# Optimization experiments

Hardware: AMD Instinct MI355X
Metric: run time of the kernel (lower is better)

The kernel has to match this reference:

```python
import jax, jax.numpy as jnp
import numpy as np

D = 128   # input_dim / num vars
LEAKY_SLOPE = 0.01  # torch F.leaky_relu default


def setup_inputs() -> dict:
    key = jax.random.key(0)
    ks = jax.random.split(key, 7)
    h, o, b = 64, 2, 8192
    scale = 0.05  # keep activations in a sane range
    return {
        "x": jax.random.normal(ks[0], (b, D), jnp.float32),
        "w0": jax.random.normal(ks[1], (D, h, D), jnp.float32) * scale,
        "w1": jax.random.normal(ks[2], (D, h, h), jnp.float32) * scale,
        "w2": jax.random.normal(ks[3], (D, o, h), jnp.float32) * scale,
        "b0": jax.random.normal(ks[4], (D, h), jnp.float32) * scale,
        "b1": jax.random.normal(ks[5], (D, h), jnp.float32) * scale,
        "b2": jax.random.normal(ks[6], (D, o), jnp.float32) * scale,
    }


def reference(x, w0, w1, w2, b0, b1, b2):
    # adjacency: all-ones minus identity (variable t cannot see itself)
    adj = jnp.ones((D, D), x.dtype) - jnp.eye(D, dtype=x.dtype)  # [j? no: (i,j)] symmetric
    # layer 0: out[b,t,i] = sum_j w0[t,i,j] * adj[j,t] * x[b,j]
    # mask the per-variable weights once, then a single contraction (no (t,i,j,b) intermediate)
    w0m = w0 * adj.T[:, None, :]            # (t,i,j); adj symmetric so adj[j,t]==adj[t,j]
    h = jnp.einsum('tij,bj->bti', w0m, x) + b0
    h = jax.nn.leaky_relu(h, LEAKY_SLOPE)
    # layer 1: per-variable dense
    h = jnp.einsum('tij,btj->bti', w1, h) + b1
    h = jax.nn.leaky_relu(h, LEAKY_SLOPE)
    # layer 2 (output, no nonlinearity)
    out = jnp.einsum('tij,btj->bti', w2, h) + b2  # (b, D, output_dim)
    # torch version returns torch.unbind(out, 1); stacked array carries same values
    return out
```

## Files before the change

### kernel.cpp

```cpp
#include <hip/hip_runtime.h>


typedef __bf16 bf16_t;
typedef __bf16 bf16x8 __attribute__((ext_vector_type(8)));
typedef float  f32x4  __attribute__((ext_vector_type(4)));

#define LEAKY 0.01f

#define XB_OFF   0u
#define W0B_OFF  (2048u*1024u)
#define W1B_OFF  (4096u*1024u)
#define W2B_OFF  (5120u*1024u)

#define W0L   0
#define W1L   16384
#define W2L   24576
#define HL    26624
#define H2L   43008
#define SMEMB 59392

__device__ __forceinline__ void async_copy16(void* lds, const void* g) {
    __builtin_amdgcn_global_load_lds(
        (const __attribute__((address_space(1))) unsigned int*)g,
        (__attribute__((address_space(3))) unsigned int*)lds, 16, 0, 0);
}

__global__ __launch_bounds__(256)
void brickify(const float* __restrict__ x,  const float* __restrict__ w0,
              const float* __restrict__ w1, const float* __restrict__ w2,
              unsigned char* __restrict__ ws)
{
    const int wid  = blockIdx.x * 4 + (threadIdx.x >> 6);
    const int lane = threadIdx.x & 63;
    const int lr = lane & 15, lq = lane >> 4;

    float v[8];
    if (wid < 2048) {
        int bt = wid >> 5, rem = wid & 31, nt = rem >> 2, ks = rem & 3;
        const float* s = x + (size_t)(bt*128 + nt*16 + lr) * 128 + ks*32 + lq*8;
        const float4 a = *(const float4*)s, b = *(const float4*)(s + 4);
        v[0]=a.x; v[1]=a.y; v[2]=a.z; v[3]=a.w;
        v[4]=b.x; v[5]=b.y; v[6]=b.z; v[7]=b.w;
    } else if (wid < 4096) {
        int u = wid - 2048, t = u >> 4, rem = u & 15, it = rem >> 2, ks = rem & 3;
        int k0 = ks*32 + lq*8;
        const float* s = w0 + (size_t)(t*64 + it*16 + lr) * 128 + k0;
        const float4 a = *(const float4*)s, b = *(const float4*)(s + 4);
        v[0]=a.x; v[1]=a.y; v[2]=a.z; v[3]=a.w;
        v[4]=b.x; v[5]=b.y; v[6]=b.z; v[7]=b.w;
        #pragma unroll
        for (int j = 0; j < 8; ++j) if (k0 + j == t) v[j] = 0.f;
    } else if (wid < 5120) {
        int u = wid - 4096, t = u >> 3, rem = u & 7, it = rem >> 1, ks = rem & 1;
        const float* s = w1 + (size_t)(t*64 + it*16 + lr) * 64 + ks*32 + lq*8;
        const float4 a = *(const float4*)s, b = *(const float4*)(s + 4);
        v[0]=a.x; v[1]=a.y; v[2]=a.z; v[3]=a.w;
        v[4]=b.x; v[5]=b.y; v[6]=b.z; v[7]=b.w;
    } else {
        int u = wid - 5120, t = u >> 1, ks = u & 1;
        #pragma unroll
        for (int j = 0; j < 8; ++j) v[j] = 0.f;
        if (lr < 2) {
            const float* s = w2 + (size_t)(t*2 + lr) * 64 + ks*32 + lq*8;
            const float4 a = *(const float4*)s, b = *(const float4*)(s + 4);
            v[0]=a.x; v[1]=a.y; v[2]=a.z; v[3]=a.w;
            v[4]=b.x; v[5]=b.y; v[6]=b.z; v[7]=b.w;
        }
    }
    union { bf16_t h[8]; uint4 q; } pk;
    #pragma unroll
    for (int j = 0; j < 8; ++j) pk.h[j] = (bf16_t)v[j];
    ((uint4*)ws)[(size_t)wid * 64 + lane] = pk.q;
}

__global__ __launch_bounds__(256, 2)
void fused_mlp(const unsigned char* __restrict__ ws,
               const float* __restrict__ b0, const float* __restrict__ b1,
               const float* __restrict__ b2, float* __restrict__ out)
{
    __shared__ __align__(1024) unsigned char smem[SMEMB];
    const int tid  = threadIdx.x;
    const int w    = tid >> 6;
    const int lane = tid & 63;
    const int lr = lane & 15, lq = lane >> 4;
    const int bt = blockIdx.x;
    const int t  = blockIdx.y;

    bf16x8 xf[2][4];
    #pragma unroll
    for (int ntl = 0; ntl < 2; ++ntl) {
        int ntg = w * 2 + ntl;
        #pragma unroll
        for (int ks = 0; ks < 4; ++ks)
            xf[ntl][ks] = *(const bf16x8*)(ws + XB_OFF
                            + (size_t)(((bt*8 + ntg)*4 + ks) * 1024) + lane*16);
    }
    f32x4 b0q[4], b1q[4];
    #pragma unroll
    for (int it = 0; it < 4; ++it) {
        b0q[it] = *(const f32x4*)(b0 + t*64 + it*16 + lq*4);
        b1q[it] = *(const f32x4*)(b1 + t*64 + it*16 + lq*4);
    }
    const float2 b2v = *(const float2*)(b2 + t*2);

    for (int c = w; c < 26; c += 4) {
        const unsigned char* g;
        if (c < 16)      g = ws + W0B_OFF + (size_t)t*16384 + c*1024;
        else if (c < 24) g = ws + W1B_OFF + (size_t)t*8192  + (c-16)*1024;
        else             g = ws + W2B_OFF + (size_t)t*2048  + (c-24)*1024;
        async_copy16(smem + c*1024 + lane*16, g + lane*16);
    }
    __syncthreads();

    bf16x8 w0f[4][4];
    #pragma unroll
    for (int it = 0; it < 4; ++it)
        #pragma unroll
        for (int ks = 0; ks < 4; ++ks)
            w0f[it][ks] = *(const bf16x8*)(smem + W0L + (it*4+ks)*1024 + lane*16);

    f32x4 acc0[2][4];
    #pragma unroll
    for (int a = 0; a < 2; ++a)
        #pragma unroll
        for (int b = 0; b < 4; ++b) acc0[a][b] = (f32x4){0.f,0.f,0.f,0.f};

    #pragma unroll
    for (int ks = 0; ks < 4; ++ks)
        #pragma unroll
        for (int it = 0; it < 4; ++it)
            #pragma unroll
            for (int ntl = 0; ntl < 2; ++ntl)
                acc0[ntl][it] = __builtin_amdgcn_mfma_f32_16x16x32_bf16(
                                    w0f[it][ks], xf[ntl][ks], acc0[ntl][it], 0, 0, 0);

    #pragma unroll
    for (int ntl = 0; ntl < 2; ++ntl)
        #pragma unroll
        for (int it = 0; it < 4; ++it) {
            union { bf16_t h[4]; unsigned long long u; } pk;
            #pragma unroll
            for (int r = 0; r < 4; ++r) {
                float u = acc0[ntl][it][r] + b0q[it][r];
                pk.h[r] = (bf16_t)(u > 0.f ? u : LEAKY * u);
            }
            int off = ((w*2+ntl)*2 + (it>>1)) * 1024
                    + (((it&1)*2 + (lq>>1))*16 + lr) * 16 + (lq&1)*8;
            *(unsigned long long*)(smem + HL + off) = pk.u;
        }

    bf16x8 w1f[4][2], hf[2][2];
    #pragma unroll
    for (int it = 0; it < 4; ++it)
        #pragma unroll
        for (int ks = 0; ks < 2; ++ks)
            w1f[it][ks] = *(const bf16x8*)(smem + W1L + (it*2+ks)*1024 + lane*16);
    #pragma unroll
    for (int ntl = 0; ntl < 2; ++ntl)
        #pragma unroll
        for (int ks = 0; ks < 2; ++ks)
            hf[ntl][ks] = *(const bf16x8*)(smem + HL + ((w*2+ntl)*2 + ks)*1024 + lane*16);

    f32x4 acc1[2][4];
    #pragma unroll
    for (int a = 0; a < 2; ++a)
        #pragma unroll
        for (int b = 0; b < 4; ++b) acc1[a][b] = (f32x4){0.f,0.f,0.f,0.f};

    #pragma unroll
    for (int ks = 0; ks < 2; ++ks)
        #pragma unroll
        for (int it = 0; it < 4; ++it)
            #pragma unroll
            for (int ntl = 0; ntl < 2; ++ntl)
                acc1[ntl][it] = __builtin_amdgcn_mfma_f32_16x16x32_bf16(
                                    w1f[it][ks], hf[ntl][ks], acc1[ntl][it], 0, 0, 0);

    #pragma unroll
    for (int ntl = 0; ntl < 2; ++ntl)
        #pragma unroll
        for (int it = 0; it < 4; ++it) {
            union { bf16_t h[4]; unsigned long long u; } pk;
            #pragma unroll
            for (int r = 0; r < 4; ++r) {
                float u = acc1[ntl][it][r] + b1q[it][r];
                pk.h[r] = (bf16_t)(u > 0.f ? u : LEAKY * u);
            }
            int off = ((w*2+ntl)*2 + (it>>1)) * 1024
                    + (((it&1)*2 + (lq>>1))*16 + lr) * 16 + (lq&1)*8;
            *(unsigned long long*)(smem + H2L + off) = pk.u;
        }

    bf16x8 w2f[2], h2f[2][2];
    #pragma unroll
    for (int ks = 0; ks < 2; ++ks)
        w2f[ks] = *(const bf16x8*)(smem + W2L + ks*1024 + lane*16);
    #pragma unroll
    for (int ntl = 0; ntl < 2; ++ntl)
        #pragma unroll
        for (int ks = 0; ks < 2; ++ks)
            h2f[ntl][ks] = *(const bf16x8*)(smem + H2L + ((w*2+ntl)*2 + ks)*1024 + lane*16);

    f32x4 acc2[2];
    acc2[0] = (f32x4){0.f,0.f,0.f,0.f};
    acc2[1] = (f32x4){0.f,0.f,0.f,0.f};
    #pragma unroll
    for (int ks = 0; ks < 2; ++ks)
        #pragma unroll
        for (int ntl = 0; ntl < 2; ++ntl)
            acc2[ntl] = __builtin_amdgcn_mfma_f32_16x16x32_bf16(
                            w2f[ks], h2f[ntl][ks], acc2[ntl], 0, 0, 0);

    if (lq == 0) {
        #pragma unroll
        for (int ntl = 0; ntl < 2; ++ntl) {
            int row = bt*128 + (w*2+ntl)*16 + lr;
            float2 o2 = { acc2[ntl][0] + b2v.x, acc2[ntl][1] + b2v.y };
            *(float2*)(out + (size_t)row*256 + t*2) = o2;
        }
    }
}

extern "C" void kernel_launch(void* const* d_in, const int* in_sizes, int n_in,
                              void* d_out, int out_size, void* d_ws, size_t ws_size,
                              hipStream_t stream) {
    const float* x  = (const float*)d_in[0];
    const float* w0 = (const float*)d_in[1];
    const float* w1 = (const float*)d_in[2];
    const float* w2 = (const float*)d_in[3];
    const float* b0 = (const float*)d_in[4];
    const float* b1 = (const float*)d_in[5];
    const float* b2 = (const float*)d_in[6];
    unsigned char* ws = (unsigned char*)d_ws;
    float* out = (float*)d_out;

    brickify<<<dim3(1344), dim3(256), 0, stream>>>(x, w0, w1, w2, ws);
    fused_mlp<<<dim3(64, 128), dim3(256), 0, stream>>>(ws, b0, b1, b2, out);
}
```

Baseline: 123.6 us.

## Keep per-variable weights in registers and loop blocks over eight batch tiles

The fused MLP kernel now loads each variable's weight fragments straight from global memory into registers once and reuses them across eight batch tiles per block. Previously every block staged the weights through LDS for a single tile. The grid shrinks from 64x128 to 8x128 blocks, and the next tile's x fragments are prefetched while the current tile computes. Biases are folded into the accumulator initialisation and leaky ReLU uses fmaxf. LDS drops to one 16 KB activation buffer, but fewer blocks means less parallelism. The higher register pressure could also cut occupancy, and reusing one LDS buffer for h and h2 without barriers relies on each wave touching only its own region.

```diff
diff --git a/kernel.cpp b/kernel.cpp
--- a/kernel.cpp
+++ b/kernel.cpp
@@ -11,19 +11,6 @@
 #define W0B_OFF  (2048u*1024u)
 #define W1B_OFF  (4096u*1024u)
 #define W2B_OFF  (5120u*1024u)
-
-#define W0L   0
-#define W1L   16384
-#define W2L   24576
-#define HL    26624
-#define H2L   43008
-#define SMEMB 59392
-
-__device__ __forceinline__ void async_copy16(void* lds, const void* g) {
-    __builtin_amdgcn_global_load_lds(
-        (const __attribute__((address_space(1))) unsigned int*)g,
-        (__attribute__((address_space(3))) unsigned int*)lds, 16, 0, 0);
-}
 
 __global__ __launch_bounds__(256)
 void brickify(const float* __restrict__ x,  const float* __restrict__ w0,
@@ -78,23 +65,33 @@
                const float* __restrict__ b0, const float* __restrict__ b1,
                const float* __restrict__ b2, float* __restrict__ out)
 {
-    __shared__ __align__(1024) unsigned char smem[SMEMB];
+    __shared__ __align__(16) unsigned char hsm[16384];
+
     const int tid  = threadIdx.x;
     const int w    = tid >> 6;
     const int lane = tid & 63;
     const int lr = lane & 15, lq = lane >> 4;
-    const int bt = blockIdx.x;
+    const int g  = blockIdx.x;
     const int t  = blockIdx.y;
 
-    bf16x8 xf[2][4];
-    #pragma unroll
-    for (int ntl = 0; ntl < 2; ++ntl) {
-        int ntg = w * 2 + ntl;
+    const unsigned char* w0p = ws + W0B_OFF + (size_t)t*16384 + lane*16;
+    const unsigned char* w1p = ws + W1B_OFF + (size_t)t*8192  + lane*16;
+    const unsigned char* w2p = ws + W2B_OFF + (size_t)t*2048  + lane*16;
+    bf16x8 w0f[4][4], w1f[4][2], w2f[2];
+    #pragma unroll
+    for (int it = 0; it < 4; ++it)
         #pragma unroll
         for (int ks = 0; ks < 4; ++ks)
-            xf[ntl][ks] = *(const bf16x8*)(ws + XB_OFF
-                            + (size_t)(((bt*8 + ntg)*4 + ks) * 1024) + lane*16);
-    }
+            w0f[it][ks] = *(const bf16x8*)(w0p + (it*4+ks)*1024);
+    #pragma unroll
+    for (int it = 0; it < 4; ++it)
+        #pragma unroll
+        for (int ks = 0; ks < 2; ++ks)
+            w1f[it][ks] = *(const bf16x8*)(w1p + (it*2+ks)*1024);
+    #pragma unroll
+    for (int ks = 0; ks < 2; ++ks)
+        w2f[ks] = *(const bf16x8*)(w2p + ks*1024);
+
     f32x4 b0q[4], b1q[4];
     #pragma unroll
     for (int it = 0; it < 4; ++it) {
@@ -103,120 +100,120 @@
     }
     const float2 b2v = *(const float2*)(b2 + t*2);
 
-    for (int c = w; c < 26; c += 4) {
-        const unsigned char* g;
-        if (c < 16)      g = ws + W0B_OFF + (size_t)t*16384 + c*1024;
-        else if (c < 24) g = ws + W1B_OFF + (size_t)t*8192  + (c-16)*1024;
-        else             g = ws + W2B_OFF + (size_t)t*2048  + (c-24)*1024;
-        async_copy16(smem + c*1024 + lane*16, g + lane*16);
-    }
-    __syncthreads();
-
-    bf16x8 w0f[4][4];
-    #pragma unroll
-    for (int it = 0; it < 4; ++it)
+    const unsigned char* xp = ws + XB_OFF + lane*16;
+    bf16x8 xf[2][4];
+    {
+        const int bt0 = g*8;
+        #pragma unroll
+        for (int ntl = 0; ntl < 2; ++ntl)
+            #pragma unroll
+            for (int ks = 0; ks < 4; ++ks)
+                xf[ntl][ks] = *(const bf16x8*)(xp + (size_t)(((bt0*8 + w*2+ntl)*4 + ks))*1024);
+    }
+
+    for (int s = 0; s < 8; ++s) {
+        const int bt = g*8 + s;
+
+        f32x4 acc0[2][4];
+        #pragma unroll
+        for (int ntl = 0; ntl < 2; ++ntl)
+            #pragma unroll
+            for (int it = 0; it < 4; ++it) acc0[ntl][it] = b0q[it];
+
         #pragma unroll
         for (int ks = 0; ks < 4; ++ks)
-            w0f[it][ks] = *(const bf16x8*)(smem + W0L + (it*4+ks)*1024 + lane*16);
-
-    f32x4 acc0[2][4];
-    #pragma unroll
-    for (int a = 0; a < 2; ++a)
-        #pragma unroll
-        for (int b = 0; b < 4; ++b) acc0[a][b] = (f32x4){0.f,0.f,0.f,0.f};
-
-    #pragma unroll
-    for (int ks = 0; ks < 4; ++ks)
-        #pragma unroll
-        for (int it = 0; it < 4; ++it)
+            #pragma unroll
+            for (int it = 0; it < 4; ++it)
+                #pragma unroll
+                for (int ntl = 0; ntl < 2; ++ntl)
+                    acc0[ntl][it] = __builtin_amdgcn_mfma_f32_16x16x32_bf16(
+                                        w0f[it][ks], xf[ntl][ks], acc0[ntl][it], 0, 0, 0);
+
+        {
+            const int btn = (s < 7) ? bt + 1 : bt;
             #pragma unroll
             for (int ntl = 0; ntl < 2; ++ntl)
-                acc0[ntl][it] = __builtin_amdgcn_mfma_f32_16x16x32_bf16(
-                                    w0f[it][ks], xf[ntl][ks], acc0[ntl][it], 0, 0, 0);
-
-    #pragma unroll
-    for (int ntl = 0; ntl < 2; ++ntl)
-        #pragma unroll
-        for (int it = 0; it < 4; ++it) {
-            union { bf16_t h[4]; unsigned long long u; } pk;
-            #pragma unroll
-            for (int r = 0; r < 4; ++r) {
-                float u = acc0[ntl][it][r] + b0q[it][r];
-                pk.h[r] = (bf16_t)(u > 0.f ? u : LEAKY * u);
+                #pragma unroll
+                for (int ks = 0; ks < 4; ++ks)
+                    xf[ntl][ks] = *(const bf16x8*)(xp + (size_t)(((btn*8 + w*2+ntl)*4 + ks))*1024);
+        }
+
+        #pragma unroll
+        for (int ntl = 0; ntl < 2; ++ntl)
+            #pragma unroll
+            for (int it = 0; it < 4; ++it) {
+                union { bf16_t h[4]; unsigned long long u; } pk;
+                #pragma unroll
+                for (int r = 0; r < 4; ++r) {
+                    float u = acc0[ntl][it][r];
+                    pk.h[r] = (bf16_t)fmaxf(u, LEAKY * u);
+                }
+                int off = ((w*2+ntl)*2 + (it>>1)) * 1024
+                        + (((it&1)*2 + (lq>>1))*16 + lr) * 16 + (lq&1)*8;
+                *(unsigned long long*)(hsm + off) = pk.u;
             }
-            int off = ((w*2+ntl)*2 + (it>>1)) * 1024
-                    + (((it&1)*2 + (lq>>1))*16 + lr) * 16 + (lq&1)*8;
-            *(unsigned long long*)(smem + HL + off) = pk.u;
-        }
-
-    bf16x8 w1f[4][2], hf[2][2];
-    #pragma unroll
-    for (int it = 0; it < 4; ++it)
+
+        bf16x8 hf[2][2];
+        #pragma unroll
+        for (int ntl = 0; ntl < 2; ++ntl)
+            #pragma unroll
+            for (int ks = 0; ks < 2; ++ks)
+                hf[ntl][ks] = *(const bf16x8*)(hsm + ((w*2+ntl)*2 + ks)*1024 + lane*16);
+
+        f32x4 acc1[2][4];
+        #pragma unroll
+        for (int ntl = 0; ntl < 2; ++ntl)
+            #pragma unroll
+            for (int it = 0; it < 4; ++it) acc1[ntl][it] = b1q[it];
+
         #pragma unroll
         for (int ks = 0; ks < 2; ++ks)
-            w1f[it][ks] = *(const bf16x8*)(smem + W1L + (it*2+ks)*1024 + lane*16);
-    #pragma unroll
-    for (int ntl = 0; ntl < 2; ++ntl)
+            #pragma unroll
+            for (int it = 0; it < 4; ++it)
+                #pragma unroll
+                for (int ntl = 0; ntl < 2; ++ntl)
+                    acc1[ntl][it] = __builtin_amdgcn_mfma_f32_16x16x32_bf16(
+                                        w1f[it][ks], hf[ntl][ks], acc1[ntl][it], 0, 0, 0);
+
+        #pragma unroll
+        for (int ntl = 0; ntl < 2; ++ntl)
+            #pragma unroll
+            for (int it = 0; it < 4; ++it) {
+                union { bf16_t h[4]; unsigned long long u; } pk;
+                #pragma unroll
+                for (int r = 0; r < 4; ++r) {
+                    float u = acc1[ntl][it][r];
+                    pk.h[r] = (bf16_t)fmaxf(u, LEAKY * u);
+                }
+                int off = ((w*2+ntl)*2 + (it>>1)) * 1024
+                        + (((it&1)*2 + (lq>>1))*16 + lr) * 16 + (lq&1)*8;
+                *(unsigned long long*)(hsm + off) = pk.u;
+            }
+
+        bf16x8 h2f[2][2];
+        #pragma unroll
+        for (int ntl = 0; ntl < 2; ++ntl)
+            #pragma unroll
+            for (int ks = 0; ks < 2; ++ks)
+                h2f[ntl][ks] = *(const bf16x8*)(hsm + ((w*2+ntl)*2 + ks)*1024 + lane*16);
+
+        f32x4 acc2[2];
+        acc2[0] = (f32x4){0.f,0.f,0.f,0.f};
+        acc2[1] = (f32x4){0.f,0.f,0.f,0.f};
         #pragma unroll
         for (int ks = 0; ks < 2; ++ks)
-            hf[ntl][ks] = *(const bf16x8*)(smem + HL + ((w*2+ntl)*2 + ks)*1024 + lane*16);
-
-    f32x4 acc1[2][4];
-    #pragma unroll
-    for (int a = 0; a < 2; ++a)
-        #pragma unroll
-        for (int b = 0; b < 4; ++b) acc1[a][b] = (f32x4){0.f,0.f,0.f,0.f};
-
-    #pragma unroll
-    for (int ks = 0; ks < 2; ++ks)
-        #pragma unroll
-        for (int it = 0; it < 4; ++it)
             #pragma unroll
             for (int ntl = 0; ntl < 2; ++ntl)
-                acc1[ntl][it] = __builtin_amdgcn_mfma_f32_16x16x32_bf16(
-                                    w1f[it][ks], hf[ntl][ks], acc1[ntl][it], 0, 0, 0);
-
-    #pragma unroll
-    for (int ntl = 0; ntl < 2; ++ntl)
-        #pragma unroll
-        for (int it = 0; it < 4; ++it) {
-            union { bf16_t h[4]; unsigned long long u; } pk;
-            #pragma unroll
-            for (int r = 0; r < 4; ++r) {
-                float u = acc1[ntl][it][r] + b1q[it][r];
-                pk.h[r] = (bf16_t)(u > 0.f ? u : LEAKY * u);
+                acc2[ntl] = __builtin_amdgcn_mfma_f32_16x16x32_bf16(
+                                w2f[ks], h2f[ntl][ks], acc2[ntl], 0, 0, 0);
+
+        if (lq == 0) {
+            #pragma unroll
+            for (int ntl = 0; ntl < 2; ++ntl) {
+                int row = bt*128 + (w*2+ntl)*16 + lr;
+                float2 o2 = { acc2[ntl][0] + b2v.x, acc2[ntl][1] + b2v.y };
+                *(float2*)(out + (size_t)row*256 + t*2) = o2;
             }
-            int off = ((w*2+ntl)*2 + (it>>1)) * 1024
-                    + (((it&1)*2 + (lq>>1))*16 + lr) * 16 + (lq&1)*8;
-            *(unsigned long long*)(smem + H2L + off) = pk.u;
-        }
-
-    bf16x8 w2f[2], h2f[2][2];
-    #pragma unroll
-    for (int ks = 0; ks < 2; ++ks)
-        w2f[ks] = *(const bf16x8*)(smem + W2L + ks*1024 + lane*16);
-    #pragma unroll
-    for (int ntl = 0; ntl < 2; ++ntl)
-        #pragma unroll
-        for (int ks = 0; ks < 2; ++ks)
-            h2f[ntl][ks] = *(const bf16x8*)(smem + H2L + ((w*2+ntl)*2 + ks)*1024 + lane*16);
-
-    f32x4 acc2[2];
-    acc2[0] = (f32x4){0.f,0.f,0.f,0.f};
-    acc2[1] = (f32x4){0.f,0.f,0.f,0.f};
-    #pragma unroll
-    for (int ks = 0; ks < 2; ++ks)
-        #pragma unroll
-        for (int ntl = 0; ntl < 2; ++ntl)
-            acc2[ntl] = __builtin_amdgcn_mfma_f32_16x16x32_bf16(
-                            w2f[ks], h2f[ntl][ks], acc2[ntl], 0, 0, 0);
-
-    if (lq == 0) {
-        #pragma unroll
-        for (int ntl = 0; ntl < 2; ++ntl) {
-            int row = bt*128 + (w*2+ntl)*16 + lr;
-            float2 o2 = { acc2[ntl][0] + b2v.x, acc2[ntl][1] + b2v.y };
-            *(float2*)(out + (size_t)row*256 + t*2) = o2;
         }
     }
 }
@@ -235,5 +232,5 @@
     float* out = (float*)d_out;
 
     brickify<<<dim3(1344), dim3(256), 0, stream>>>(x, w0, w1, w2, ws);
-    fused_mlp<<<dim3(64, 128), dim3(256), 0, stream>>>(ws, b0, b1, b2, out);
+    fused_mlp<<<dim3(8, 128), dim3(256), 0, stream>>>(ws, b0, b1, b2, out);
 }
```

New measurement: 107.4 us. 13.1% less time.
